# Kernel tuning notes

Hardware: AMD Instinct MI355X
Metric: run time of the kernel (lower is better)

The kernel has to match this reference:

```python
import jax, jax.numpy as jnp
import numpy as np

B, INPUT_DIM, EMB_DIM = 16384, 2048, 768
DOMAIN_NUM, MEMORY_NUM, TAU = 9, 10, 32.0


def setup_inputs() -> dict:
    key = jax.random.key(0)
    k1, k2, k3, k4, k5 = jax.random.split(key, 5)
    feature = jax.random.normal(k1, (B, INPUT_DIM), dtype=jnp.float32)
    category = jax.random.randint(k2, (B,), 0, DOMAIN_NUM, dtype=jnp.int64)
    # Linear(input_dim, emb_dim, bias=False) weights: [emb_dim, input_dim]
    W_topic = jax.random.normal(k3, (EMB_DIM, INPUT_DIM), dtype=jnp.float32) * 0.02
    W_domain = jax.random.normal(k4, (EMB_DIM, INPUT_DIM), dtype=jnp.float32) * 0.02
    # domain_num Embedding(memory_num, emb_dim) tables, stacked: [D, M, E]
    memory_tables = jax.random.normal(k5, (DOMAIN_NUM, MEMORY_NUM, EMB_DIM), dtype=jnp.float32)
    return {"feature": feature, "W_topic": W_topic, "W_domain": W_domain,
            "memory_tables": memory_tables, "category": category}


def reference(feature, W_topic, W_domain, memory_tables, category):
    eps = 1e-12
    # F.normalize(feature, p=2, dim=-1)
    norm = jnp.maximum(jnp.linalg.norm(feature, axis=-1, keepdims=True), eps)
    feat = feature / norm                                   # [B, I]
    # per-sample gather of each sample's category memory table: [B, M, E]
    mem = memory_tables[category]
    # faithful quirk: loop over domain_num indexes the BATCH dim of the stack
    D = memory_tables.shape[0]
    mems_d = mem[:D]                                        # [D, M, E]
    t = feat @ W_topic.T                                    # [B, E]
    topic_att = jax.nn.softmax(jnp.einsum('be,dme->bdm', t, mems_d) * TAU, axis=-1)
    sep = jnp.einsum('bdm,dme->bde', topic_att, mems_d)     # [B, D, E]
    dproj = feat @ W_domain.T                               # [B, E]
    domain_att = jax.nn.softmax(jnp.einsum('bde,be->bd', sep, dproj) * TAU, axis=-1)
    return domain_att[:, None, :]                           # [B, 1, D]
```

## Files before the change

kernel.cpp:

```cpp
#include <hip/hip_runtime.h>
#include <math.h>

#define TAU_F 32.0f

typedef __attribute__((ext_vector_type(8))) _Float16 half8;
typedef __attribute__((ext_vector_type(2))) __fp16 half2v;
typedef __attribute__((ext_vector_type(4))) float f32x4;

union HU { uint4 u; half8 v; };

__device__ __forceinline__ void sync_lds_only() {
    asm volatile("s_waitcnt lgkmcnt(0)" ::: "memory");
    __builtin_amdgcn_s_barrier();
}

__global__ __launch_bounds__(256) void gproj2(
    const float* __restrict__ Wt, const float* __restrict__ Wd,
    const float* __restrict__ mem, const int* __restrict__ cat,
    float* __restrict__ P)
{
    __shared__ float Ml[96 * 36];
    __shared__ float Wl[32 * 68];

    const int bid = blockIdx.x;
    const int mat = bid >> 7;
    const int ks  = (bid >> 5) & 3;
    const int ct  = bid & 31;
    const int c0  = ct * 64;
    const int tid = threadIdx.x;
    const float* __restrict__ W = mat ? Wd : Wt;

    const int tr = tid >> 4;
    const int tc = tid & 15;

    float acc[6][4];
    #pragma unroll
    for (int j = 0; j < 6; ++j)
        #pragma unroll
        for (int q = 0; q < 4; ++q) acc[j][q] = 0.f;

    for (int ch = 0; ch < 6; ++ch) {
        __syncthreads();
        #pragma unroll
        for (int p = 0; p < 3; ++p) {
            const int idx = tid + 256 * p;
            const int r   = idx >> 3;
            const int kq  = idx & 7;
            float4 v = make_float4(0.f, 0.f, 0.f, 0.f);
            if (r < 90) {
                const int d = r / 10;
                const int mrow = cat[d] * 10 + (r - d * 10);
                v = *(const float4*)(mem + (size_t)mrow * 768 + ks * 192 + ch * 32 + kq * 4);
            }
            *(float4*)(Ml + r * 36 + kq * 4) = v;
        }
        #pragma unroll
        for (int p = 0; p < 2; ++p) {
            const int idx = tid + 256 * p;
            const int e   = idx >> 4;
            const int c4  = (idx & 15) * 4;
            *(float4*)(Wl + e * 68 + c4) =
                *(const float4*)(W + (size_t)(ks * 192 + ch * 32 + e) * 2048 + c0 + c4);
        }
        __syncthreads();

        #pragma unroll
        for (int e = 0; e < 32; e += 4) {
            float4 m4[6], w4[4];
            #pragma unroll
            for (int j = 0; j < 6; ++j) m4[j] = *(const float4*)(Ml + (tr * 6 + j) * 36 + e);
            #pragma unroll
            for (int q = 0; q < 4; ++q) w4[q] = *(const float4*)(Wl + (e + q) * 68 + tc * 4);
            #pragma unroll
            for (int j = 0; j < 6; ++j) {
                const float mv[4] = {m4[j].x, m4[j].y, m4[j].z, m4[j].w};
                #pragma unroll
                for (int q = 0; q < 4; ++q) {
                    acc[j][0] = fmaf(mv[q], w4[q].x, acc[j][0]);
                    acc[j][1] = fmaf(mv[q], w4[q].y, acc[j][1]);
                    acc[j][2] = fmaf(mv[q], w4[q].z, acc[j][2]);
                    acc[j][3] = fmaf(mv[q], w4[q].w, acc[j][3]);
                }
            }
        }
    }

    #pragma unroll
    for (int j = 0; j < 6; ++j) {
        float4 v = make_float4(acc[j][0], acc[j][1], acc[j][2], acc[j][3]);
        *(float4*)(P + (size_t)ks * 393216 + (size_t)(mat * 96 + tr * 6 + j) * 2048 + c0 + tc * 4) = v;
    }
}

__global__ __launch_bounds__(256) void split_g3(
    const float* __restrict__ P, unsigned short* __restrict__ gB)
{
    const int u  = blockIdx.x * 256 + threadIdx.x;
    const int n  = u >> 8;
    const int k0 = (u & 255) * 8;

    float s[8] = {0.f, 0.f, 0.f, 0.f, 0.f, 0.f, 0.f, 0.f};
    #pragma unroll
    for (int ks = 0; ks < 4; ++ks) {
        const float4 a = *(const float4*)(P + (size_t)ks * 393216 + (size_t)n * 2048 + k0);
        const float4 b = *(const float4*)(P + (size_t)ks * 393216 + (size_t)n * 2048 + k0 + 4);
        s[0] += a.x; s[1] += a.y; s[2] += a.z; s[3] += a.w;
        s[4] += b.x; s[5] += b.y; s[6] += b.z; s[7] += b.w;
    }
    union { _Float16 h[8]; uint4 u4; } hi, lo;
    #pragma unroll
    for (int e = 0; e < 8; ++e) {
        const _Float16 h = (_Float16)s[e];
        hi.h[e] = h;
        lo.h[e] = (_Float16)(s[e] - (float)h);
    }
    const int kc = k0 >> 5;
    const int lq = (k0 >> 3) & 3;
    const int nq = n / 48;
    const int rm = n - nq * 48;
    const int j  = rm >> 4;
    const int lm = rm & 15;
    const size_t fH = (size_t)((kc * 12 + nq * 3 + j) * 2 + 0) * 512 + lq * 128 + lm * 8;
    const size_t fL = (size_t)((kc * 12 + nq * 3 + j) * 2 + 1) * 512 + lq * 128 + lm * 8;
    *(uint4*)(gB + fH) = hi.u4;
    *(uint4*)(gB + fL) = lo.u4;
}

__global__ __launch_bounds__(256, 2) void fused_ep(
    const float* __restrict__ feat, const unsigned short* __restrict__ gB,
    float* __restrict__ out)
{
    __shared__ __align__(16) unsigned char smraw[32 * 193 * 4];
    unsigned short* aS = (unsigned short*)smraw;
    float* sc = (float*)smraw;
    __shared__ float ssqS[32];

    const int tid  = threadIdx.x;
    const int row0 = blockIdx.x * 32;

    const int w  = tid >> 6, l = tid & 63;
    const int lm = l & 15,  lq = l >> 4;
    const bool roleT = (w < 2);
    const int cf0 = 2 * w;
    const int tf  = 2 + w;
    const int db  = 6 + (w - 2) * 3;
    const int sr = tid >> 3, kq = tid & 7;
    const int skf = kq >> 2, sk4 = kq & 3;

    f32x4 acc[2][4];
    #pragma unroll
    for (int i = 0; i < 2; ++i)
        #pragma unroll
        for (int j = 0; j < 4; ++j) acc[i][j] = (f32x4)0.f;
    float ssq = 0.f;

    const float* fbase = feat + (size_t)(row0 + sr) * 2048 + kq * 8;
    const unsigned short* lB = gB + l * 8;

    auto cw = [&](int buf, float4 va, float4 vb) {
        const float xs[8] = {va.x, va.y, va.z, va.w, vb.x, vb.y, vb.z, vb.w};
        union { half2v h2[4]; uint4 u4; } uh, ul;
        #pragma unroll
        for (int e = 0; e < 4; ++e) {
            const float a = xs[2 * e], b = xs[2 * e + 1];
            ssq = fmaf(a, a, ssq); ssq = fmaf(b, b, ssq);
            half2v h = __builtin_amdgcn_cvt_pkrtz(a, b);
            uh.h2[e] = h;
            ul.h2[e] = __builtin_amdgcn_cvt_pkrtz(a - (float)h[0], b - (float)h[1]);
        }
        *(uint4*)(aS + (size_t)(((buf * 2 + 0) * 2 + skf) * 32 + sr) * 40 + sk4 * 8) = uh.u4;
        *(uint4*)(aS + (size_t)(((buf * 2 + 1) * 2 + skf) * 32 + sr) * 40 + sk4 * 8) = ul.u4;
    };

    float4 c0a = *(const float4*)(fbase);
    float4 c0b = *(const float4*)(fbase + 4);
    float4 c1a = *(const float4*)(fbase + 64);
    float4 c1b = *(const float4*)(fbase + 68);
    cw(0, c0a, c0b);
    sync_lds_only();

    for (int kt = 0; kt < 32; ++kt) {
        uint4 bA[2], bB[2], bC[2], bD[2], bE[2];
        if (roleT) {
            #pragma unroll
            for (int kf = 0; kf < 2; ++kf) {
                const unsigned short* p = lB + (size_t)((2 * kt + kf) * 12 + cf0) * 1024;
                bA[kf] = *(const uint4*)(p);
                bB[kf] = *(const uint4*)(p + 512);
                bC[kf] = *(const uint4*)(p + 1024);
                bD[kf] = *(const uint4*)(p + 1536);
            }
        } else {
            #pragma unroll
            for (int kf = 0; kf < 2; ++kf) {
                const unsigned short* pt = lB + (size_t)((2 * kt + kf) * 12 + tf) * 1024;
                bA[kf] = *(const uint4*)(pt);
                bB[kf] = *(const uint4*)(pt + 512);
                const unsigned short* pd = lB + (size_t)((2 * kt + kf) * 12 + db) * 1024;
                bC[kf] = *(const uint4*)(pd);
                bD[kf] = *(const uint4*)(pd + 1024);
                bE[kf] = *(const uint4*)(pd + 2048);
            }
        }
        const int ka = (kt + 2 < 32) ? kt + 2 : 31;
        float4 cna = *(const float4*)(fbase + ka * 64);
        float4 cnb = *(const float4*)(fbase + ka * 64 + 4);

        if (kt < 31) cw((kt + 1) & 1, c1a, c1b);

        const int cb = kt & 1;
        half8 fh[2][2], fl[2][2];
        #pragma unroll
        for (int i = 0; i < 2; ++i)
            #pragma unroll
            for (int kf = 0; kf < 2; ++kf) {
                HU th, tl;
                th.u = *(const uint4*)(aS + (size_t)(((cb * 2 + 0) * 2 + kf) * 32 + i * 16 + lm) * 40 + lq * 8);
                tl.u = *(const uint4*)(aS + (size_t)(((cb * 2 + 1) * 2 + kf) * 32 + i * 16 + lm) * 40 + lq * 8);
                fh[i][kf] = th.v;
                fl[i][kf] = tl.v;
            }

        if (roleT) {
            #pragma unroll
            for (int kf = 0; kf < 2; ++kf)
                #pragma unroll
                for (int i = 0; i < 2; ++i) {
                    HU hA, hB, hC, hD;
                    hA.u = bA[kf]; hB.u = bB[kf]; hC.u = bC[kf]; hD.u = bD[kf];
                    acc[i][0] = __builtin_amdgcn_mfma_f32_16x16x32_f16(fh[i][kf], hA.v, acc[i][0], 0, 0, 0);
                    acc[i][0] = __builtin_amdgcn_mfma_f32_16x16x32_f16(fh[i][kf], hB.v, acc[i][0], 0, 0, 0);
                    acc[i][0] = __builtin_amdgcn_mfma_f32_16x16x32_f16(fl[i][kf], hA.v, acc[i][0], 0, 0, 0);
                    acc[i][1] = __builtin_amdgcn_mfma_f32_16x16x32_f16(fh[i][kf], hC.v, acc[i][1], 0, 0, 0);
                    acc[i][1] = __builtin_amdgcn_mfma_f32_16x16x32_f16(fh[i][kf], hD.v, acc[i][1], 0, 0, 0);
                    acc[i][1] = __builtin_amdgcn_mfma_f32_16x16x32_f16(fl[i][kf], hC.v, acc[i][1], 0, 0, 0);
                }
        } else {
            #pragma unroll
            for (int kf = 0; kf < 2; ++kf)
                #pragma unroll
                for (int i = 0; i < 2; ++i) {
                    HU hA, hB, hC, hD, hE;
                    hA.u = bA[kf]; hB.u = bB[kf]; hC.u = bC[kf]; hD.u = bD[kf]; hE.u = bE[kf];
                    acc[i][0] = __builtin_amdgcn_mfma_f32_16x16x32_f16(fh[i][kf], hA.v, acc[i][0], 0, 0, 0);
                    acc[i][0] = __builtin_amdgcn_mfma_f32_16x16x32_f16(fh[i][kf], hB.v, acc[i][0], 0, 0, 0);
                    acc[i][0] = __builtin_amdgcn_mfma_f32_16x16x32_f16(fl[i][kf], hA.v, acc[i][0], 0, 0, 0);
                    acc[i][1] = __builtin_amdgcn_mfma_f32_16x16x32_f16(fh[i][kf], hC.v, acc[i][1], 0, 0, 0);
                    acc[i][2] = __builtin_amdgcn_mfma_f32_16x16x32_f16(fh[i][kf], hD.v, acc[i][2], 0, 0, 0);
                    acc[i][3] = __builtin_amdgcn_mfma_f32_16x16x32_f16(fh[i][kf], hE.v, acc[i][3], 0, 0, 0);
                }
        }

        sync_lds_only();
        c1a = cna; c1b = cnb;
    }

    if (roleT) {
        #pragma unroll
        for (int i = 0; i < 2; ++i)
            #pragma unroll
            for (int f = 0; f < 2; ++f)
                #pragma unroll
                for (int r4 = 0; r4 < 4; ++r4)
                    sc[(i * 16 + lq * 4 + r4) * 193 + (cf0 + f) * 16 + lm] = acc[i][f][r4];
    } else {
        #pragma unroll
        for (int i = 0; i < 2; ++i)
            #pragma unroll
            for (int f = 0; f < 4; ++f) {
                const int cf = (f == 0) ? tf : (db + f - 1);
                #pragma unroll
                for (int r4 = 0; r4 < 4; ++r4)
                    sc[(i * 16 + lq * 4 + r4) * 193 + cf * 16 + lm] = acc[i][f][r4];
            }
    }

    ssq += __shfl_xor(ssq, 1, 64);
    ssq += __shfl_xor(ssq, 2, 64);
    ssq += __shfl_xor(ssq, 4, 64);
    if (kq == 0) ssqS[sr] = ssq;
    __syncthreads();

    if (tid < 64) {
        const int r  = tid >> 1, hf = tid & 1;
        const int nd = hf ? 4 : 5;
        const int d0 = hf ? 5 : 0;
        const float inv = TAU_F / fmaxf(sqrtf(ssqS[r]), 1e-12f);
        const float* scr = sc + (size_t)r * 193;
        float lg[5];
        float dmax = -1e30f;
        #pragma unroll
        for (int dd = 0; dd < 5; ++dd) {
            if (dd < nd) {
                const int d = d0 + dd;
                const float* v = scr + d * 10;
                const float* u = scr + 96 + d * 10;
                float mx = v[0];
                #pragma unroll
                for (int m = 1; m < 10; ++m) mx = fmaxf(mx, v[m]);
                float ssum = 0.f, dot = 0.f;
                #pragma unroll
                for (int m = 0; m < 10; ++m) {
                    const float p = __expf((v[m] - mx) * inv);
                    ssum += p;
                    dot = fmaf(p, u[m], dot);
                }
                const float lgt = (dot / ssum) * inv;
                lg[dd] = lgt;
                dmax = fmaxf(dmax, lgt);
            } else {
                lg[dd] = -1e30f;
            }
        }
        dmax = fmaxf(dmax, __shfl_xor(dmax, 1, 64));
        float s2 = 0.f;
        #pragma unroll
        for (int dd = 0; dd < 5; ++dd) {
            const float p = __expf(lg[dd] - dmax);
            lg[dd] = p;
            s2 += p;
        }
        s2 += __shfl_xor(s2, 1, 64);
        const float r2 = 1.0f / s2;
        #pragma unroll
        for (int dd = 0; dd < 5; ++dd)
            if (dd < nd)
                out[(size_t)(row0 + r) * 9 + d0 + dd] = lg[dd] * r2;
    }
}

extern "C" void kernel_launch(void* const* d_in, const int* in_sizes, int n_in,
                              void* d_out, int out_size, void* d_ws, size_t ws_size,
                              hipStream_t stream) {
    const float* feature = (const float*)d_in[0];
    const float* Wt      = (const float*)d_in[1];
    const float* Wd      = (const float*)d_in[2];
    const float* mem     = (const float*)d_in[3];
    const int*   cat     = (const int*)d_in[4];

    float* P  = (float*)d_ws;
    unsigned short* gB = (unsigned short*)((char*)d_ws + 50331648);
    float* out = (float*)d_out;

    gproj2<<<256, 256, 0, stream>>>(Wt, Wd, mem, cat, P);
    split_g3<<<192, 256, 0, stream>>>(P, gB);
    fused_ep<<<512, 256, 0, stream>>>(feature, gB, out);
}
```

Measured before the change: 248.1 us.

## Stage B fragments in LDS and share them across 64-row blocks

The fused epilogue kernel now processes 64 rows per block with 512 threads instead of 32 rows with 256. The split-precision B fragments for the next k-tile are cooperatively loaded from global memory into a double-buffered LDS area, so two row-groups of waves reuse each B tile. This is meant to halve redundant global/L2 traffic for the projection weights and to hide that traffic behind the current tile's MFMAs. In exchange LDS use rises to about 112 KB per block, which may limit how many blocks can be resident on a CU, and each iteration adds LDS writes.

```diff
diff --git a/kernel.cpp b/kernel.cpp
--- a/kernel.cpp
+++ b/kernel.cpp
@@ -126,24 +126,29 @@
     *(uint4*)(gB + fL) = lo.u4;
 }
 
-__global__ __launch_bounds__(256, 2) void fused_ep(
+__global__ __launch_bounds__(512, 2) void fused_ep(
     const float* __restrict__ feat, const unsigned short* __restrict__ gB,
     float* __restrict__ out)
 {
-    __shared__ __align__(16) unsigned char smraw[32 * 193 * 4];
+    __shared__ __align__(16) unsigned char smraw[114688];
     unsigned short* aS = (unsigned short*)smraw;
+    unsigned short* Bl = (unsigned short*)(smraw + 40960);
     float* sc = (float*)smraw;
-    __shared__ float ssqS[32];
+    __shared__ float ssqS[64];
 
     const int tid  = threadIdx.x;
-    const int row0 = blockIdx.x * 32;
+    const int row0 = blockIdx.x * 64;
 
     const int w  = tid >> 6, l = tid & 63;
     const int lm = l & 15,  lq = l >> 4;
-    const bool roleT = (w < 2);
-    const int cf0 = 2 * w;
-    const int tf  = 2 + w;
-    const int db  = 6 + (w - 2) * 3;
+    const int iw = w >> 2;
+    const int r  = w & 3;
+    const bool roleT = (r < 2);
+    const int f0 = 4 * r;
+    const int tf = 2 + r;
+    const int tp = 2 * tf;
+    const int dp = 12 + 3 * (r - 2);
+    const int db = 6 + 3 * (r - 2);
     const int sr = tid >> 3, kq = tid & 7;
     const int skf = kq >> 2, sk4 = kq & 3;
 
@@ -155,7 +160,29 @@
     float ssq = 0.f;
 
     const float* fbase = feat + (size_t)(row0 + sr) * 2048 + kq * 8;
-    const unsigned short* lB = gB + l * 8;
+
+    auto loadB = [&](int kt2, uint4* bn) {
+        #pragma unroll
+        for (int s = 0; s < 5; ++s) {
+            const int p = w + 8 * s;
+            if (p < 36) {
+                const int kf = (p >= 18) ? 1 : 0;
+                const int fi = p - kf * 18;
+                const int cf = (fi < 12) ? (fi >> 1) : (fi - 6);
+                const int pl = (fi < 12) ? (fi & 1) : 0;
+                bn[s] = *(const uint4*)(gB + (size_t)(((2 * kt2 + kf) * 12 + cf) * 1024)
+                                           + pl * 512 + l * 8);
+            }
+        }
+    };
+    auto writeB = [&](int buf, const uint4* bn) {
+        #pragma unroll
+        for (int s = 0; s < 5; ++s) {
+            const int p = w + 8 * s;
+            if (p < 36)
+                *(uint4*)(Bl + ((size_t)buf * 36 + p) * 512 + l * 8) = bn[s];
+        }
+    };
 
     auto cw = [&](int buf, float4 va, float4 vb) {
         const float xs[8] = {va.x, va.y, va.z, va.w, vb.x, vb.y, vb.z, vb.w};
@@ -168,88 +195,86 @@
             uh.h2[e] = h;
             ul.h2[e] = __builtin_amdgcn_cvt_pkrtz(a - (float)h[0], b - (float)h[1]);
         }
-        *(uint4*)(aS + (size_t)(((buf * 2 + 0) * 2 + skf) * 32 + sr) * 40 + sk4 * 8) = uh.u4;
-        *(uint4*)(aS + (size_t)(((buf * 2 + 1) * 2 + skf) * 32 + sr) * 40 + sk4 * 8) = ul.u4;
+        *(uint4*)(aS + (size_t)(((buf * 2 + 0) * 2 + skf) * 64 + sr) * 40 + sk4 * 8) = uh.u4;
+        *(uint4*)(aS + (size_t)(((buf * 2 + 1) * 2 + skf) * 64 + sr) * 40 + sk4 * 8) = ul.u4;
     };
 
-    float4 c0a = *(const float4*)(fbase);
-    float4 c0b = *(const float4*)(fbase + 4);
+    {
+        uint4 b0[5];
+        loadB(0, b0);
+        float4 c0a = *(const float4*)(fbase);
+        float4 c0b = *(const float4*)(fbase + 4);
+        cw(0, c0a, c0b);
+        writeB(0, b0);
+    }
     float4 c1a = *(const float4*)(fbase + 64);
     float4 c1b = *(const float4*)(fbase + 68);
-    cw(0, c0a, c0b);
     sync_lds_only();
 
     for (int kt = 0; kt < 32; ++kt) {
-        uint4 bA[2], bB[2], bC[2], bD[2], bE[2];
-        if (roleT) {
-            #pragma unroll
-            for (int kf = 0; kf < 2; ++kf) {
-                const unsigned short* p = lB + (size_t)((2 * kt + kf) * 12 + cf0) * 1024;
-                bA[kf] = *(const uint4*)(p);
-                bB[kf] = *(const uint4*)(p + 512);
-                bC[kf] = *(const uint4*)(p + 1024);
-                bD[kf] = *(const uint4*)(p + 1536);
-            }
-        } else {
-            #pragma unroll
-            for (int kf = 0; kf < 2; ++kf) {
-                const unsigned short* pt = lB + (size_t)((2 * kt + kf) * 12 + tf) * 1024;
-                bA[kf] = *(const uint4*)(pt);
-                bB[kf] = *(const uint4*)(pt + 512);
-                const unsigned short* pd = lB + (size_t)((2 * kt + kf) * 12 + db) * 1024;
-                bC[kf] = *(const uint4*)(pd);
-                bD[kf] = *(const uint4*)(pd + 1024);
-                bE[kf] = *(const uint4*)(pd + 2048);
-            }
-        }
+        const int cb = kt & 1;
+        uint4 bn[5];
+        if (kt < 31) loadB(kt + 1, bn);
         const int ka = (kt + 2 < 32) ? kt + 2 : 31;
         float4 cna = *(const float4*)(fbase + ka * 64);
         float4 cnb = *(const float4*)(fbase + ka * 64 + 4);
-
         if (kt < 31) cw((kt + 1) & 1, c1a, c1b);
 
-        const int cb = kt & 1;
         half8 fh[2][2], fl[2][2];
         #pragma unroll
-        for (int i = 0; i < 2; ++i)
+        for (int ii = 0; ii < 2; ++ii)
             #pragma unroll
             for (int kf = 0; kf < 2; ++kf) {
+                const int row = (iw * 2 + ii) * 16 + lm;
                 HU th, tl;
-                th.u = *(const uint4*)(aS + (size_t)(((cb * 2 + 0) * 2 + kf) * 32 + i * 16 + lm) * 40 + lq * 8);
-                tl.u = *(const uint4*)(aS + (size_t)(((cb * 2 + 1) * 2 + kf) * 32 + i * 16 + lm) * 40 + lq * 8);
-                fh[i][kf] = th.v;
-                fl[i][kf] = tl.v;
+                th.u = *(const uint4*)(aS + (size_t)(((cb * 2 + 0) * 2 + kf) * 64 + row) * 40 + lq * 8);
+                tl.u = *(const uint4*)(aS + (size_t)(((cb * 2 + 1) * 2 + kf) * 64 + row) * 40 + lq * 8);
+                fh[ii][kf] = th.v;
+                fl[ii][kf] = tl.v;
             }
 
         if (roleT) {
             #pragma unroll
-            for (int kf = 0; kf < 2; ++kf)
-                #pragma unroll
-                for (int i = 0; i < 2; ++i) {
-                    HU hA, hB, hC, hD;
-                    hA.u = bA[kf]; hB.u = bB[kf]; hC.u = bC[kf]; hD.u = bD[kf];
-                    acc[i][0] = __builtin_amdgcn_mfma_f32_16x16x32_f16(fh[i][kf], hA.v, acc[i][0], 0, 0, 0);
-                    acc[i][0] = __builtin_amdgcn_mfma_f32_16x16x32_f16(fh[i][kf], hB.v, acc[i][0], 0, 0, 0);
-                    acc[i][0] = __builtin_amdgcn_mfma_f32_16x16x32_f16(fl[i][kf], hA.v, acc[i][0], 0, 0, 0);
-                    acc[i][1] = __builtin_amdgcn_mfma_f32_16x16x32_f16(fh[i][kf], hC.v, acc[i][1], 0, 0, 0);
-                    acc[i][1] = __builtin_amdgcn_mfma_f32_16x16x32_f16(fh[i][kf], hD.v, acc[i][1], 0, 0, 0);
-                    acc[i][1] = __builtin_amdgcn_mfma_f32_16x16x32_f16(fl[i][kf], hC.v, acc[i][1], 0, 0, 0);
+            for (int kf = 0; kf < 2; ++kf) {
+                const unsigned short* bp = Bl + ((size_t)cb * 36 + kf * 18) * 512 + l * 8;
+                HU hA, hB, hC, hD;
+                hA.u = *(const uint4*)(bp + (size_t)(f0 + 0) * 512);
+                hB.u = *(const uint4*)(bp + (size_t)(f0 + 1) * 512);
+                hC.u = *(const uint4*)(bp + (size_t)(f0 + 2) * 512);
+                hD.u = *(const uint4*)(bp + (size_t)(f0 + 3) * 512);
+                #pragma unroll
+                for (int ii = 0; ii < 2; ++ii) {
+                    acc[ii][0] = __builtin_amdgcn_mfma_f32_16x16x32_f16(fh[ii][kf], hA.v, acc[ii][0], 0, 0, 0);
+                    acc[ii][0] = __builtin_amdgcn_mfma_f32_16x16x32_f16(fh[ii][kf], hB.v, acc[ii][0], 0, 0, 0);
+                    acc[ii][0] = __builtin_amdgcn_mfma_f32_16x16x32_f16(fl[ii][kf], hA.v, acc[ii][0], 0, 0, 0);
+                    acc[ii][1] = __builtin_amdgcn_mfma_f32_16x16x32_f16(fh[ii][kf], hC.v, acc[ii][1], 0, 0, 0);
+                    acc[ii][1] = __builtin_amdgcn_mfma_f32_16x16x32_f16(fh[ii][kf], hD.v, acc[ii][1], 0, 0, 0);
+                    acc[ii][1] = __builtin_amdgcn_mfma_f32_16x16x32_f16(fl[ii][kf], hC.v, acc[ii][1], 0, 0, 0);
                 }
+            }
         } else {
             #pragma unroll
-            for (int kf = 0; kf < 2; ++kf)
-                #pragma unroll
-                for (int i = 0; i < 2; ++i) {
-                    HU hA, hB, hC, hD, hE;
-                    hA.u = bA[kf]; hB.u = bB[kf]; hC.u = bC[kf]; hD.u = bD[kf]; hE.u = bE[kf];
-                    acc[i][0] = __builtin_amdgcn_mfma_f32_16x16x32_f16(fh[i][kf], hA.v, acc[i][0], 0, 0, 0);
-                    acc[i][0] = __builtin_amdgcn_mfma_f32_16x16x32_f16(fh[i][kf], hB.v, acc[i][0], 0, 0, 0);
-                    acc[i][0] = __builtin_amdgcn_mfma_f32_16x16x32_f16(fl[i][kf], hA.v, acc[i][0], 0, 0, 0);
-                    acc[i][1] = __builtin_amdgcn_mfma_f32_16x16x32_f16(fh[i][kf], hC.v, acc[i][1], 0, 0, 0);
-                    acc[i][2] = __builtin_amdgcn_mfma_f32_16x16x32_f16(fh[i][kf], hD.v, acc[i][2], 0, 0, 0);
-                    acc[i][3] = __builtin_amdgcn_mfma_f32_16x16x32_f16(fh[i][kf], hE.v, acc[i][3], 0, 0, 0);
+            for (int kf = 0; kf < 2; ++kf) {
+                const unsigned short* bp = Bl + ((size_t)cb * 36 + kf * 18) * 512 + l * 8;
+                HU hA, hB, hC, hD, hE;
+                hA.u = *(const uint4*)(bp + (size_t)(tp + 0) * 512);
+                hB.u = *(const uint4*)(bp + (size_t)(tp + 1) * 512);
+                hC.u = *(const uint4*)(bp + (size_t)(dp + 0) * 512);
+                hD.u = *(const uint4*)(bp + (size_t)(dp + 1) * 512);
+                hE.u = *(const uint4*)(bp + (size_t)(dp + 2) * 512);
+                #pragma unroll
+                for (int ii = 0; ii < 2; ++ii) {
+                    acc[ii][0] = __builtin_amdgcn_mfma_f32_16x16x32_f16(fh[ii][kf], hA.v, acc[ii][0], 0, 0, 0);
+                    acc[ii][0] = __builtin_amdgcn_mfma_f32_16x16x32_f16(fh[ii][kf], hB.v, acc[ii][0], 0, 0, 0);
+                    acc[ii][0] = __builtin_amdgcn_mfma_f32_16x16x32_f16(fl[ii][kf], hA.v, acc[ii][0], 0, 0, 0);
+                    acc[ii][1] = __builtin_amdgcn_mfma_f32_16x16x32_f16(fh[ii][kf], hC.v, acc[ii][1], 0, 0, 0);
+                    acc[ii][2] = __builtin_amdgcn_mfma_f32_16x16x32_f16(fh[ii][kf], hD.v, acc[ii][2], 0, 0, 0);
+                    acc[ii][3] = __builtin_amdgcn_mfma_f32_16x16x32_f16(fh[ii][kf], hE.v, acc[ii][3], 0, 0, 0);
                 }
-        }
+            }
+        }
+
+        if (kt < 31) writeB((kt + 1) & 1, bn);
 
         sync_lds_only();
         c1a = cna; c1b = cnb;
@@ -257,21 +282,21 @@
 
     if (roleT) {
         #pragma unroll
-        for (int i = 0; i < 2; ++i)
+        for (int ii = 0; ii < 2; ++ii)
             #pragma unroll
             for (int f = 0; f < 2; ++f)
                 #pragma unroll
                 for (int r4 = 0; r4 < 4; ++r4)
-                    sc[(i * 16 + lq * 4 + r4) * 193 + (cf0 + f) * 16 + lm] = acc[i][f][r4];
+                    sc[((iw * 2 + ii) * 16 + lq * 4 + r4) * 193 + (2 * r + f) * 16 + lm] = acc[ii][f][r4];
     } else {
         #pragma unroll
-        for (int i = 0; i < 2; ++i)
+        for (int ii = 0; ii < 2; ++ii)
             #pragma unroll
             for (int f = 0; f < 4; ++f) {
                 const int cf = (f == 0) ? tf : (db + f - 1);
                 #pragma unroll
                 for (int r4 = 0; r4 < 4; ++r4)
-                    sc[(i * 16 + lq * 4 + r4) * 193 + cf * 16 + lm] = acc[i][f][r4];
+                    sc[((iw * 2 + ii) * 16 + lq * 4 + r4) * 193 + cf * 16 + lm] = acc[ii][f][r4];
             }
     }
 
@@ -281,12 +306,12 @@
     if (kq == 0) ssqS[sr] = ssq;
     __syncthreads();
 
-    if (tid < 64) {
-        const int r  = tid >> 1, hf = tid & 1;
+    if (tid < 128) {
+        const int rr = tid >> 1, hf = tid & 1;
         const int nd = hf ? 4 : 5;
         const int d0 = hf ? 5 : 0;
-        const float inv = TAU_F / fmaxf(sqrtf(ssqS[r]), 1e-12f);
-        const float* scr = sc + (size_t)r * 193;
+        const float inv = TAU_F / fmaxf(sqrtf(ssqS[rr]), 1e-12f);
+        const float* scr = sc + (size_t)rr * 193;
         float lg[5];
         float dmax = -1e30f;
         #pragma unroll
@@ -325,7 +350,7 @@
         #pragma unroll
         for (int dd = 0; dd < 5; ++dd)
             if (dd < nd)
-                out[(size_t)(row0 + r) * 9 + d0 + dd] = lg[dd] * r2;
+                out[(size_t)(row0 + rr) * 9 + d0 + dd] = lg[dd] * r2;
     }
 }
 
@@ -344,5 +369,5 @@
 
     gproj2<<<256, 256, 0, stream>>>(Wt, Wd, mem, cat, P);
     split_g3<<<192, 256, 0, stream>>>(P, gB);
-    fused_ep<<<512, 256, 0, stream>>>(feature, gB, out);
-}
+    fused_ep<<<256, 512, 0, stream>>>(feature, gB, out);
+}
```

After: 261.7 us. 1.05x slower.

## Halve rows per block in fused epilogue and prefetch B fragments a step ahead

Applied to the files above, without the earlier changes.

The fused GEMM+softmax kernel now processes 16 rows per block instead of 32, doubling the grid to 1024 blocks and raising launch bounds to allow 4 blocks per CU. Per-thread accumulators and A-fragments shrink. B-fragment global loads are moved after the MFMAs so the next iteration's B tile is prefetched into registers. This is meant to improve occupancy and hide global-load latency. In exchange, each B fragment loaded from global memory is reused across half as many rows, which doubles B traffic through L2.

```diff
diff --git a/kernel.cpp b/kernel.cpp
--- a/kernel.cpp
+++ b/kernel.cpp
@@ -8,6 +8,7 @@
 typedef __attribute__((ext_vector_type(4))) float f32x4;
 
 union HU { uint4 u; half8 v; };
+union H2U { half2v h; unsigned int u; };
 
 __device__ __forceinline__ void sync_lds_only() {
     asm volatile("s_waitcnt lgkmcnt(0)" ::: "memory");
@@ -126,167 +127,160 @@
     *(uint4*)(gB + fL) = lo.u4;
 }
 
-__global__ __launch_bounds__(256, 2) void fused_ep(
+__global__ __launch_bounds__(256, 4) void fused_ep(
     const float* __restrict__ feat, const unsigned short* __restrict__ gB,
     float* __restrict__ out)
 {
-    __shared__ __align__(16) unsigned char smraw[32 * 193 * 4];
+    __shared__ __align__(16) unsigned char smraw[12352];
     unsigned short* aS = (unsigned short*)smraw;
     float* sc = (float*)smraw;
-    __shared__ float ssqS[32];
+    __shared__ float ssqS[16];
 
     const int tid  = threadIdx.x;
-    const int row0 = blockIdx.x * 32;
+    const int row0 = blockIdx.x * 16;
 
     const int w  = tid >> 6, l = tid & 63;
     const int lm = l & 15,  lq = l >> 4;
     const bool roleT = (w < 2);
     const int cf0 = 2 * w;
     const int tf  = 2 + w;
-    const int db  = 6 + (w - 2) * 3;
-    const int sr = tid >> 3, kq = tid & 7;
-    const int skf = kq >> 2, sk4 = kq & 3;
-
-    f32x4 acc[2][4];
-    #pragma unroll
-    for (int i = 0; i < 2; ++i)
-        #pragma unroll
-        for (int j = 0; j < 4; ++j) acc[i][j] = (f32x4)0.f;
+    const int db  = 6 + 3 * (w - 2);
+    const int sr = tid >> 4, kq = tid & 15;
+    const int skf = kq >> 3, sk4 = kq & 7;
+
+    f32x4 acc[4];
+    #pragma unroll
+    for (int j = 0; j < 4; ++j) acc[j] = (f32x4)0.f;
     float ssq = 0.f;
 
-    const float* fbase = feat + (size_t)(row0 + sr) * 2048 + kq * 8;
+    const float* fbase = feat + (size_t)(row0 + sr) * 2048 + kq * 4;
     const unsigned short* lB = gB + l * 8;
 
-    auto cw = [&](int buf, float4 va, float4 vb) {
-        const float xs[8] = {va.x, va.y, va.z, va.w, vb.x, vb.y, vb.z, vb.w};
-        union { half2v h2[4]; uint4 u4; } uh, ul;
-        #pragma unroll
-        for (int e = 0; e < 4; ++e) {
-            const float a = xs[2 * e], b = xs[2 * e + 1];
-            ssq = fmaf(a, a, ssq); ssq = fmaf(b, b, ssq);
-            half2v h = __builtin_amdgcn_cvt_pkrtz(a, b);
-            uh.h2[e] = h;
-            ul.h2[e] = __builtin_amdgcn_cvt_pkrtz(a - (float)h[0], b - (float)h[1]);
-        }
-        *(uint4*)(aS + (size_t)(((buf * 2 + 0) * 2 + skf) * 32 + sr) * 40 + sk4 * 8) = uh.u4;
-        *(uint4*)(aS + (size_t)(((buf * 2 + 1) * 2 + skf) * 32 + sr) * 40 + sk4 * 8) = ul.u4;
+    auto cw = [&](int buf, float4 v) {
+        ssq = fmaf(v.x, v.x, ssq); ssq = fmaf(v.y, v.y, ssq);
+        ssq = fmaf(v.z, v.z, ssq); ssq = fmaf(v.w, v.w, ssq);
+        H2U h0, h1, l0, l1;
+        h0.h = __builtin_amdgcn_cvt_pkrtz(v.x, v.y);
+        h1.h = __builtin_amdgcn_cvt_pkrtz(v.z, v.w);
+        l0.h = __builtin_amdgcn_cvt_pkrtz(v.x - (float)h0.h[0], v.y - (float)h0.h[1]);
+        l1.h = __builtin_amdgcn_cvt_pkrtz(v.z - (float)h1.h[0], v.w - (float)h1.h[1]);
+        uint2 hi; hi.x = h0.u; hi.y = h1.u;
+        uint2 lo; lo.x = l0.u; lo.y = l1.u;
+        *(uint2*)(aS + (size_t)(((buf * 2 + 0) * 2 + skf) * 16 + sr) * 40 + sk4 * 4) = hi;
+        *(uint2*)(aS + (size_t)(((buf * 2 + 1) * 2 + skf) * 16 + sr) * 40 + sk4 * 4) = lo;
     };
 
-    float4 c0a = *(const float4*)(fbase);
-    float4 c0b = *(const float4*)(fbase + 4);
-    float4 c1a = *(const float4*)(fbase + 64);
-    float4 c1b = *(const float4*)(fbase + 68);
-    cw(0, c0a, c0b);
+    auto loadB = [&](int kt, uint4 b[2][5]) {
+        #pragma unroll
+        for (int kf = 0; kf < 2; ++kf) {
+            const unsigned short* bk = lB + (size_t)(2 * kt + kf) * 12288;
+            if (roleT) {
+                const unsigned short* p = bk + (size_t)cf0 * 1024;
+                b[kf][0] = *(const uint4*)(p);
+                b[kf][1] = *(const uint4*)(p + 512);
+                b[kf][2] = *(const uint4*)(p + 1024);
+                b[kf][3] = *(const uint4*)(p + 1536);
+            } else {
+                const unsigned short* pt = bk + (size_t)tf * 1024;
+                b[kf][0] = *(const uint4*)(pt);
+                b[kf][1] = *(const uint4*)(pt + 512);
+                const unsigned short* pd = bk + (size_t)db * 1024;
+                b[kf][2] = *(const uint4*)(pd);
+                b[kf][3] = *(const uint4*)(pd + 1024);
+                b[kf][4] = *(const uint4*)(pd + 2048);
+            }
+        }
+    };
+
+    uint4  b[2][5];
+    {
+        float4 c0 = *(const float4*)(fbase);
+        loadB(0, b);
+        cw(0, c0);
+    }
+    float4 c1 = *(const float4*)(fbase + 64);
     sync_lds_only();
 
     for (int kt = 0; kt < 32; ++kt) {
-        uint4 bA[2], bB[2], bC[2], bD[2], bE[2];
+        const int cb = kt & 1;
+
+        if (kt < 31) cw((kt + 1) & 1, c1);
+
+        half8 fh[2], fl[2];
+        #pragma unroll
+        for (int kf = 0; kf < 2; ++kf) {
+            HU th, tl;
+            th.u = *(const uint4*)(aS + (size_t)(((cb * 2 + 0) * 2 + kf) * 16 + lm) * 40 + lq * 8);
+            tl.u = *(const uint4*)(aS + (size_t)(((cb * 2 + 1) * 2 + kf) * 16 + lm) * 40 + lq * 8);
+            fh[kf] = th.v;
+            fl[kf] = tl.v;
+        }
+
         if (roleT) {
             #pragma unroll
             for (int kf = 0; kf < 2; ++kf) {
-                const unsigned short* p = lB + (size_t)((2 * kt + kf) * 12 + cf0) * 1024;
-                bA[kf] = *(const uint4*)(p);
-                bB[kf] = *(const uint4*)(p + 512);
-                bC[kf] = *(const uint4*)(p + 1024);
-                bD[kf] = *(const uint4*)(p + 1536);
+                HU hA, hB, hC, hD;
+                hA.u = b[kf][0]; hB.u = b[kf][1]; hC.u = b[kf][2]; hD.u = b[kf][3];
+                acc[0] = __builtin_amdgcn_mfma_f32_16x16x32_f16(fh[kf], hA.v, acc[0], 0, 0, 0);
+                acc[0] = __builtin_amdgcn_mfma_f32_16x16x32_f16(fh[kf], hB.v, acc[0], 0, 0, 0);
+                acc[0] = __builtin_amdgcn_mfma_f32_16x16x32_f16(fl[kf], hA.v, acc[0], 0, 0, 0);
+                acc[1] = __builtin_amdgcn_mfma_f32_16x16x32_f16(fh[kf], hC.v, acc[1], 0, 0, 0);
+                acc[1] = __builtin_amdgcn_mfma_f32_16x16x32_f16(fh[kf], hD.v, acc[1], 0, 0, 0);
+                acc[1] = __builtin_amdgcn_mfma_f32_16x16x32_f16(fl[kf], hC.v, acc[1], 0, 0, 0);
             }
         } else {
             #pragma unroll
             for (int kf = 0; kf < 2; ++kf) {
-                const unsigned short* pt = lB + (size_t)((2 * kt + kf) * 12 + tf) * 1024;
-                bA[kf] = *(const uint4*)(pt);
-                bB[kf] = *(const uint4*)(pt + 512);
-                const unsigned short* pd = lB + (size_t)((2 * kt + kf) * 12 + db) * 1024;
-                bC[kf] = *(const uint4*)(pd);
-                bD[kf] = *(const uint4*)(pd + 1024);
-                bE[kf] = *(const uint4*)(pd + 2048);
-            }
-        }
-        const int ka = (kt + 2 < 32) ? kt + 2 : 31;
-        float4 cna = *(const float4*)(fbase + ka * 64);
-        float4 cnb = *(const float4*)(fbase + ka * 64 + 4);
-
-        if (kt < 31) cw((kt + 1) & 1, c1a, c1b);
-
-        const int cb = kt & 1;
-        half8 fh[2][2], fl[2][2];
-        #pragma unroll
-        for (int i = 0; i < 2; ++i)
-            #pragma unroll
-            for (int kf = 0; kf < 2; ++kf) {
-                HU th, tl;
-                th.u = *(const uint4*)(aS + (size_t)(((cb * 2 + 0) * 2 + kf) * 32 + i * 16 + lm) * 40 + lq * 8);
-                tl.u = *(const uint4*)(aS + (size_t)(((cb * 2 + 1) * 2 + kf) * 32 + i * 16 + lm) * 40 + lq * 8);
-                fh[i][kf] = th.v;
-                fl[i][kf] = tl.v;
-            }
-
-        if (roleT) {
-            #pragma unroll
-            for (int kf = 0; kf < 2; ++kf)
-                #pragma unroll
-                for (int i = 0; i < 2; ++i) {
-                    HU hA, hB, hC, hD;
-                    hA.u = bA[kf]; hB.u = bB[kf]; hC.u = bC[kf]; hD.u = bD[kf];
-                    acc[i][0] = __builtin_amdgcn_mfma_f32_16x16x32_f16(fh[i][kf], hA.v, acc[i][0], 0, 0, 0);
-                    acc[i][0] = __builtin_amdgcn_mfma_f32_16x16x32_f16(fh[i][kf], hB.v, acc[i][0], 0, 0, 0);
-                    acc[i][0] = __builtin_amdgcn_mfma_f32_16x16x32_f16(fl[i][kf], hA.v, acc[i][0], 0, 0, 0);
-                    acc[i][1] = __builtin_amdgcn_mfma_f32_16x16x32_f16(fh[i][kf], hC.v, acc[i][1], 0, 0, 0);
-                    acc[i][1] = __builtin_amdgcn_mfma_f32_16x16x32_f16(fh[i][kf], hD.v, acc[i][1], 0, 0, 0);
-                    acc[i][1] = __builtin_amdgcn_mfma_f32_16x16x32_f16(fl[i][kf], hC.v, acc[i][1], 0, 0, 0);
-                }
-        } else {
-            #pragma unroll
-            for (int kf = 0; kf < 2; ++kf)
-                #pragma unroll
-                for (int i = 0; i < 2; ++i) {
-                    HU hA, hB, hC, hD, hE;
-                    hA.u = bA[kf]; hB.u = bB[kf]; hC.u = bC[kf]; hD.u = bD[kf]; hE.u = bE[kf];
-                    acc[i][0] = __builtin_amdgcn_mfma_f32_16x16x32_f16(fh[i][kf], hA.v, acc[i][0], 0, 0, 0);
-                    acc[i][0] = __builtin_amdgcn_mfma_f32_16x16x32_f16(fh[i][kf], hB.v, acc[i][0], 0, 0, 0);
-                    acc[i][0] = __builtin_amdgcn_mfma_f32_16x16x32_f16(fl[i][kf], hA.v, acc[i][0], 0, 0, 0);
-                    acc[i][1] = __builtin_amdgcn_mfma_f32_16x16x32_f16(fh[i][kf], hC.v, acc[i][1], 0, 0, 0);
-                    acc[i][2] = __builtin_amdgcn_mfma_f32_16x16x32_f16(fh[i][kf], hD.v, acc[i][2], 0, 0, 0);
-                    acc[i][3] = __builtin_amdgcn_mfma_f32_16x16x32_f16(fh[i][kf], hE.v, acc[i][3], 0, 0, 0);
-                }
+                HU hA, hB, hC, hD, hE;
+                hA.u = b[kf][0]; hB.u = b[kf][1]; hC.u = b[kf][2];
+                hD.u = b[kf][3]; hE.u = b[kf][4];
+                acc[0] = __builtin_amdgcn_mfma_f32_16x16x32_f16(fh[kf], hA.v, acc[0], 0, 0, 0);
+                acc[0] = __builtin_amdgcn_mfma_f32_16x16x32_f16(fh[kf], hB.v, acc[0], 0, 0, 0);
+                acc[0] = __builtin_amdgcn_mfma_f32_16x16x32_f16(fl[kf], hA.v, acc[0], 0, 0, 0);
+                acc[1] = __builtin_amdgcn_mfma_f32_16x16x32_f16(fh[kf], hC.v, acc[1], 0, 0, 0);
+                acc[2] = __builtin_amdgcn_mfma_f32_16x16x32_f16(fh[kf], hD.v, acc[2], 0, 0, 0);
+                acc[3] = __builtin_amdgcn_mfma_f32_16x16x32_f16(fh[kf], hE.v, acc[3], 0, 0, 0);
+            }
+        }
+
+        if (kt < 31) {
+            loadB(kt + 1, b);
+            const int ka = (kt + 2 < 32) ? kt + 2 : 31;
+            c1 = *(const float4*)(fbase + ka * 64);
         }
 
         sync_lds_only();
-        c1a = cna; c1b = cnb;
     }
 
     if (roleT) {
         #pragma unroll
-        for (int i = 0; i < 2; ++i)
-            #pragma unroll
-            for (int f = 0; f < 2; ++f)
-                #pragma unroll
-                for (int r4 = 0; r4 < 4; ++r4)
-                    sc[(i * 16 + lq * 4 + r4) * 193 + (cf0 + f) * 16 + lm] = acc[i][f][r4];
+        for (int f = 0; f < 2; ++f)
+            #pragma unroll
+            for (int r4 = 0; r4 < 4; ++r4)
+                sc[(lq * 4 + r4) * 193 + (cf0 + f) * 16 + lm] = acc[f][r4];
     } else {
         #pragma unroll
-        for (int i = 0; i < 2; ++i)
-            #pragma unroll
-            for (int f = 0; f < 4; ++f) {
-                const int cf = (f == 0) ? tf : (db + f - 1);
-                #pragma unroll
-                for (int r4 = 0; r4 < 4; ++r4)
-                    sc[(i * 16 + lq * 4 + r4) * 193 + cf * 16 + lm] = acc[i][f][r4];
-            }
+        for (int f = 0; f < 4; ++f) {
+            const int cf = (f == 0) ? tf : (db + f - 1);
+            #pragma unroll
+            for (int r4 = 0; r4 < 4; ++r4)
+                sc[(lq * 4 + r4) * 193 + cf * 16 + lm] = acc[f][r4];
+        }
     }
 
     ssq += __shfl_xor(ssq, 1, 64);
     ssq += __shfl_xor(ssq, 2, 64);
     ssq += __shfl_xor(ssq, 4, 64);
-    if (kq == 0) ssqS[sr] = ssq;
+    ssq += __shfl_xor(ssq, 8, 64);
+    if ((l & 15) == 0) ssqS[w * 4 + (l >> 4)] = ssq;
     __syncthreads();
 
-    if (tid < 64) {
-        const int r  = tid >> 1, hf = tid & 1;
+    if (tid < 32) {
+        const int rr = tid >> 1, hf = tid & 1;
         const int nd = hf ? 4 : 5;
         const int d0 = hf ? 5 : 0;
-        const float inv = TAU_F / fmaxf(sqrtf(ssqS[r]), 1e-12f);
-        const float* scr = sc + (size_t)r * 193;
+        const float inv = TAU_F / fmaxf(sqrtf(ssqS[rr]), 1e-12f);
+        const float* scr = sc + (size_t)rr * 193;
         float lg[5];
         float dmax = -1e30f;
         #pragma unroll
@@ -325,7 +319,7 @@
         #pragma unroll
         for (int dd = 0; dd < 5; ++dd)
             if (dd < nd)
-                out[(size_t)(row0 + r) * 9 + d0 + dd] = lg[dd] * r2;
+                out[(size_t)(row0 + rr) * 9 + d0 + dd] = lg[dd] * r2;
     }
 }
 
@@ -344,5 +338,5 @@
 
     gproj2<<<256, 256, 0, stream>>>(Wt, Wd, mem, cat, P);
     split_g3<<<192, 256, 0, stream>>>(P, gB);
-    fused_ep<<<512, 256, 0, stream>>>(feature, gB, out);
-}
+    fused_ep<<<1024, 256, 0, stream>>>(feature, gB, out);
+}
```

Result: slower. 661.4 us (+166.6%).
